# Kernel optimization log

Measured on AMD Instinct MI355X. Metric: run time of the kernel, lower is better.

## Reference

```python
import jax, jax.numpy as jnp
import numpy as np

B, S, C_IN = 32, 4096, 21
D_MODEL = 512
M, TAU = 7, 1
K = M + 1                 # kernel_size = 8
NUM_KERNELS = 74          # 73 depthwise kernels + 1 'final' kernel
PAD = M * TAU             # left zero-pad = 7 -> num_windows == S
PROJ_IN = 73 * C_IN + 1   # 1534


def setup_inputs() -> dict:
    key = jax.random.key(0)
    k_x, k_k, k_w, k_b = jax.random.split(key, 4)
    x = jax.random.normal(k_x, (B, S, C_IN), dtype=jnp.float32)
    kernels = jax.random.normal(k_k, (NUM_KERNELS, K), dtype=jnp.float32)
    # nn.Conv1d(PROJ_IN, D_MODEL, 1): weight [D_MODEL, PROJ_IN, 1] -> squeeze kernel dim
    fan_in = PROJ_IN
    bound = 1.0 / np.sqrt(fan_in)
    proj_w = jax.random.uniform(k_w, (D_MODEL, PROJ_IN), dtype=jnp.float32, minval=-bound, maxval=bound)
    proj_b = jax.random.uniform(k_b, (D_MODEL,), dtype=jnp.float32, minval=-bound, maxval=bound)
    return {"x": x, "kernels": kernels, "proj_w": proj_w, "proj_b": proj_b}


def reference(x, kernels, proj_w, proj_b):
    # x: [B, S, C]. Left-pad the time axis with zeros (ConstantPad1d((PAD, 0), 0)).
    xp = jnp.pad(x, ((0, 0), (PAD, 0), (0, 0)))  # [B, S+PAD, C]
    num_windows = x.shape[1]  # (S+PAD) - K + 1 == S when tau == 1
    # Gather sliding windows: [B, W, K, C]
    idx = jnp.arange(num_windows)[:, None] * TAU + jnp.arange(K)[None, :]
    windows = xp[:, idx, :]
    # 73 depthwise kernels, each applied to every channel. Torch concat order is
    # per-kernel blocks of c_in channels: [k0 c0..cC, k1 c0..cC, ...].
    main = jnp.einsum('bwkc,nk->bwnc', windows, kernels[: NUM_KERNELS - 1])
    main = main.reshape(x.shape[0], num_windows, (NUM_KERNELS - 1) * x.shape[2])
    # Final feature: last kernel applied to one channel (torch uses a random
    # channel; fixed to channel 0 here for determinism).
    final = jnp.einsum('bwk,k->bw', windows[:, :, :, 0], kernels[NUM_KERNELS - 1])[..., None]
    combined = jnp.concatenate([main, final], axis=2)  # [B, W, 73*C+1]
    # 1x1 Conv1d projection over channels -> [B, D_MODEL, W]
    out = jnp.einsum('bwc,dc->bdw', combined, proj_w) + proj_b[None, :, None]
    return out
```

## Files before the change

### kernel.cpp

```cpp
#include <hip/hip_runtime.h>

#define B_    32
#define S_    4096
#define CIN   21
#define DM    512
#define KW    8
#define NK    74
#define PROJIN 1534
#define CP    24
#define KSEG  192

#define WT    256
#define DTB   128
#define SROWS 263
#define R_    265

typedef __attribute__((ext_vector_type(8))) short bf16x8;
typedef __attribute__((ext_vector_type(4))) float f32x4;

__device__ __forceinline__ unsigned short f2bf_rne(float x) {
  unsigned u = __float_as_uint(x);
  unsigned r = (u + 0x7FFFu + ((u >> 16) & 1u)) >> 16;
  return (unsigned short)r;
}
__device__ __forceinline__ float bf2f(unsigned short b) {
  return __uint_as_float(((unsigned)b) << 16);
}

__global__ __launch_bounds__(256) void build_weff(
    const float* __restrict__ kernels, const float* __restrict__ proj_w,
    unsigned short* __restrict__ wh, unsigned short* __restrict__ wl) {
  __shared__ float pw[PROJIN];
  __shared__ float kk[NK * KW];
  const int d = blockIdx.x, tid = threadIdx.x;
  for (int i = tid; i < PROJIN; i += 256) pw[i] = proj_w[d * PROJIN + i];
  for (int i = tid; i < NK * KW; i += 256) kk[i] = kernels[i];
  __syncthreads();
  if (tid < KSEG) {
    const int k = tid / CP, c = tid % CP;
    float acc = 0.f;
    if (c < CIN) {
      #pragma unroll 1
      for (int n = 0; n < 73; ++n)
        acc = fmaf(pw[n * CIN + c], kk[n * KW + k], acc);
      if (c == 0) acc = fmaf(pw[PROJIN - 1], kk[73 * KW + k], acc);
    }
    const unsigned short h = f2bf_rne(acc);
    wh[d * KSEG + tid] = h;
    wl[d * KSEG + tid] = f2bf_rne(acc - bf2f(h));
  }
}

__global__ __launch_bounds__(256, 2) void conv_mfma2(
    const float* __restrict__ x, const unsigned short* __restrict__ wh,
    const unsigned short* __restrict__ wl, const float* __restrict__ proj_b,
    float* __restrict__ out) {
  __shared__ __align__(16) unsigned short Xt[2 * 3 * R_ * 8];

  const int tid = threadIdx.x;
  const int blk = blockIdx.x;
  const int dt = blk & 3;
  const int wt = (blk >> 2) & 15;
  const int b  = blk >> 6;
  const int d0 = dt * DTB;
  const int w0 = wt * WT;

  const float* xb = x + (size_t)b * (S_ * CIN);
  for (int i = tid; i < SROWS * CP; i += 256) {
    const int s = i / CP, c = i - s * CP;
    const int wg = w0 - 7 + s;
    float v = 0.f;
    if (c < CIN && wg >= 0) v = xb[wg * CIN + c];
    const unsigned short h = f2bf_rne(v);
    const unsigned short lo = f2bf_rne(v - bf2f(h));
    const int g = c >> 3, e = c & 7;
    Xt[(g * R_ + s) * 8 + e] = h;
    Xt[((3 + g) * R_ + s) * 8 + e] = lo;
  }
  __syncthreads();

  const int l    = tid & 63;
  const int wave = tid >> 6;
  const int l15  = l & 15;
  const int q    = l >> 4;
  const int q8   = q * 8;

  int koff[6];
  #pragma unroll
  for (int s = 0; s < 6; ++s) {
    const int k0 = 32 * s + q8;
    const int k = k0 / CP, c0 = k0 - k * CP;
    koff[s] = (c0 >> 3) * R_ + k;
  }
  const int rowb = wave * 64 + l15;
  const int wrow = (d0 + l15) * KSEG + q8;

  f32x4 acc[4][8] = {};

  #pragma unroll
  for (int s = 0; s < 6; ++s) {
    bf16x8 fh[4], fl[4];
    #pragma unroll
    for (int m = 0; m < 4; ++m) {
      const int gi = koff[s] + rowb + m * 16;
      fh[m] = *(const bf16x8*)&Xt[gi * 8];
      fl[m] = *(const bf16x8*)&Xt[(gi + 3 * R_) * 8];
    }
    #pragma unroll
    for (int half = 0; half < 2; ++half) {
      bf16x8 fwh[4], fwl[4];
      #pragma unroll
      for (int j = 0; j < 4; ++j) {
        const int n = half * 4 + j;
        const int off = wrow + n * (16 * KSEG) + s * 32;
        fwh[j] = *(const bf16x8*)&wh[off];
        fwl[j] = *(const bf16x8*)&wl[off];
      }
      #pragma unroll
      for (int m = 0; m < 4; ++m)
        #pragma unroll
        for (int j = 0; j < 4; ++j) {
          const int n = half * 4 + j;
          acc[m][n] = __builtin_amdgcn_mfma_f32_16x16x32_bf16(
              fh[m], fwh[j], acc[m][n], 0, 0, 0);
          acc[m][n] = __builtin_amdgcn_mfma_f32_16x16x32_bf16(
              fl[m], fwh[j], acc[m][n], 0, 0, 0);
          acc[m][n] = __builtin_amdgcn_mfma_f32_16x16x32_bf16(
              fh[m], fwl[j], acc[m][n], 0, 0, 0);
        }
    }
  }

  const size_t ob = (size_t)b * DM * S_;
  #pragma unroll
  for (int n = 0; n < 8; ++n) {
    const int d = d0 + n * 16 + l15;
    const float bias = proj_b[d];
    #pragma unroll
    for (int m = 0; m < 4; ++m) {
      const int w = w0 + wave * 64 + m * 16 + q * 4;
      f32x4 v = acc[m][n];
      v = v + bias;
      *(f32x4*)&out[ob + (size_t)d * S_ + w] = v;
    }
  }
}

extern "C" void kernel_launch(void* const* d_in, const int* in_sizes, int n_in,
                              void* d_out, int out_size, void* d_ws, size_t ws_size,
                              hipStream_t stream) {
  const float* x       = (const float*)d_in[0];
  const float* kernels = (const float*)d_in[1];
  const float* proj_w  = (const float*)d_in[2];
  const float* proj_b  = (const float*)d_in[3];
  float* out = (float*)d_out;

  unsigned short* weff_hi = (unsigned short*)d_ws;
  unsigned short* weff_lo = weff_hi + (size_t)DM * KSEG;

  build_weff<<<DM, 256, 0, stream>>>(kernels, proj_w, weff_hi, weff_lo);
  conv_mfma2<<<B_ * 16 * 4, 256, 0, stream>>>(x, weff_hi, weff_lo, proj_b, out);
}
```

Baseline: 418.0 us.

## Pre-split X into bf16 hi/lo image and stream chunks via LDS-direct loads

Adds a separate pass that converts x into a padded bf16 hi/lo, channel-grouped image in global memory, and lays the effective weights out in an LDS-ready tiled image. The conv kernel now uses persistent 512-thread blocks, each owning one batch and 32 output channels. Each block loads its weight tile once and loops over 8 time chunks, fetching each X chunk with global_load_lds so the next chunk's load overlaps the output stores. Blocks are mapped for XCD locality and outputs use nontemporal stores. The extra preprocessing pass writes and rereads a bf16 copy of x. Each block also does less MFMA work per loaded X element, since it now covers 32 instead of 128 output channels.

Measured after the change: 346.8 us. -17.0%, faster.

```diff
diff --git a/kernel.cpp b/kernel.cpp
--- a/kernel.cpp
+++ b/kernel.cpp
@@ -8,36 +8,44 @@
 #define NK    74
 #define PROJIN 1534
 #define CP    24
-#define KSEG  192
 
-#define WT    256
-#define DTB   128
-#define SROWS 263
-#define R_    265
+#define DTB   32
+#define CW    512
+#define NCH   8
+#define ROWCH 519
+#define ROWP  4104
+#define WGRAN 1584
+#define XGRAN (6*ROWCH)
 
 typedef __attribute__((ext_vector_type(8))) short bf16x8;
 typedef __attribute__((ext_vector_type(4))) float f32x4;
 
 __device__ __forceinline__ unsigned short f2bf_rne(float x) {
   unsigned u = __float_as_uint(x);
-  unsigned r = (u + 0x7FFFu + ((u >> 16) & 1u)) >> 16;
-  return (unsigned short)r;
+  return (unsigned short)((u + 0x7FFFu + ((u >> 16) & 1u)) >> 16);
 }
 __device__ __forceinline__ float bf2f(unsigned short b) {
   return __uint_as_float(((unsigned)b) << 16);
 }
 
-__global__ __launch_bounds__(256) void build_weff(
+#define MFMA16 __builtin_amdgcn_mfma_f32_16x16x32_bf16
+#define GLOAD16(gsrc, ldst)                                              \
+  __builtin_amdgcn_global_load_lds(                                      \
+      (const __attribute__((address_space(1))) unsigned int*)(gsrc),     \
+      (__attribute__((address_space(3))) unsigned int*)(ldst), 16, 0, 0)
+
+__global__ __launch_bounds__(256) void build_weff3(
     const float* __restrict__ kernels, const float* __restrict__ proj_w,
-    unsigned short* __restrict__ wh, unsigned short* __restrict__ wl) {
+    unsigned short* __restrict__ wimg) {
   __shared__ float pw[PROJIN];
   __shared__ float kk[NK * KW];
   const int d = blockIdx.x, tid = threadIdx.x;
   for (int i = tid; i < PROJIN; i += 256) pw[i] = proj_w[d * PROJIN + i];
   for (int i = tid; i < NK * KW; i += 256) kk[i] = kernels[i];
   __syncthreads();
-  if (tid < KSEG) {
-    const int k = tid / CP, c = tid % CP;
+  if (tid < 192) {
+    const int kap = tid;
+    const int k = kap / CP, c = kap - k * CP;
     float acc = 0.f;
     if (c < CIN) {
       #pragma unroll 1
@@ -46,102 +54,124 @@
       if (c == 0) acc = fmaf(pw[PROJIN - 1], kk[73 * KW + k], acc);
     }
     const unsigned short h = f2bf_rne(acc);
-    wh[d * KSEG + tid] = h;
-    wl[d * KSEG + tid] = f2bf_rne(acc - bf2f(h));
+    const unsigned short lo = f2bf_rne(acc - bf2f(h));
+    const int s = kap >> 5, q = (kap >> 3) & 3, e = kap & 7;
+    const size_t base = (size_t)(d >> 5) * WGRAN * 8;
+    const int dloc = d & 31;
+    wimg[base + ((size_t)((s * 4 + q) * 33 + dloc)) * 8 + e] = h;
+    wimg[base + ((size_t)(((6 + s) * 4 + q) * 33 + dloc)) * 8 + e] = lo;
   }
 }
 
-__global__ __launch_bounds__(256, 2) void conv_mfma2(
-    const float* __restrict__ x, const unsigned short* __restrict__ wh,
-    const unsigned short* __restrict__ wl, const float* __restrict__ proj_b,
-    float* __restrict__ out) {
-  __shared__ __align__(16) unsigned short Xt[2 * 3 * R_ * 8];
+__global__ __launch_bounds__(256) void build_xt(
+    const float* __restrict__ x, unsigned short* __restrict__ xt) {
+  const int t = blockIdx.x * 256 + threadIdx.x;
+  const int b = t / (6 * ROWP);
+  int rem = t - b * 6 * ROWP;
+  const int pg = rem / ROWP;
+  const int row = rem - pg * ROWP;
+  const int h = pg / 3, g = pg % 3;
+  const int w = row - 7;
+  bf16x8 o;
+  #pragma unroll
+  for (int e = 0; e < 8; ++e) {
+    const int c = g * 8 + e;
+    float v = 0.f;
+    if (w >= 0 && w < S_ && c < CIN) v = x[((size_t)b * S_ + w) * CIN + c];
+    const unsigned short hi = f2bf_rne(v);
+    o[e] = (short)(h ? f2bf_rne(v - bf2f(hi)) : hi);
+  }
+  *(bf16x8*)&xt[(size_t)t * 8] = o;
+}
+
+__global__ __launch_bounds__(512, 4) void conv3(
+    const unsigned short* __restrict__ wimg,
+    const unsigned short* __restrict__ xt,
+    const float* __restrict__ proj_b, float* __restrict__ out) {
+  extern __shared__ __align__(16) char smem[];
+  unsigned short* Xl = (unsigned short*)smem;
+  unsigned short* Wl = (unsigned short*)(smem + XGRAN * 16);
 
   const int tid = threadIdx.x;
-  const int blk = blockIdx.x;
-  const int dt = blk & 3;
-  const int wt = (blk >> 2) & 15;
-  const int b  = blk >> 6;
+  const int p = blockIdx.x;
+  const int xcd = p & 7, slot = p >> 3;
+  const int b = xcd * 4 + (slot >> 4);
+  const int dt = slot & 15;
   const int d0 = dt * DTB;
-  const int w0 = wt * WT;
 
-  const float* xb = x + (size_t)b * (S_ * CIN);
-  for (int i = tid; i < SROWS * CP; i += 256) {
-    const int s = i / CP, c = i - s * CP;
-    const int wg = w0 - 7 + s;
-    float v = 0.f;
-    if (c < CIN && wg >= 0) v = xb[wg * CIN + c];
-    const unsigned short h = f2bf_rne(v);
-    const unsigned short lo = f2bf_rne(v - bf2f(h));
-    const int g = c >> 3, e = c & 7;
-    Xt[(g * R_ + s) * 8 + e] = h;
-    Xt[((3 + g) * R_ + s) * 8 + e] = lo;
+  const unsigned short* wsrc = wimg + (size_t)dt * WGRAN * 8;
+  for (int i = tid; i < WGRAN; i += 512)
+    GLOAD16(wsrc + (size_t)i * 8, Wl + (size_t)i * 8);
+  const unsigned short* xb = xt + (size_t)b * 6 * ROWP * 8;
+  for (int i = tid; i < XGRAN; i += 512) {
+    const int pg = i / ROWCH, r = i - pg * ROWCH;
+    GLOAD16(xb + ((size_t)pg * ROWP + r) * 8, Xl + (size_t)i * 8);
   }
-  __syncthreads();
 
-  const int l    = tid & 63;
-  const int wave = tid >> 6;
-  const int l15  = l & 15;
-  const int q    = l >> 4;
-  const int q8   = q * 8;
+  const int l = tid & 63;
+  const int wg = tid >> 6;
+  const int l15 = l & 15;
+  const int q = l >> 4;
+  const int q8 = q * 8;
 
   int koff[6];
   #pragma unroll
   for (int s = 0; s < 6; ++s) {
     const int k0 = 32 * s + q8;
     const int k = k0 / CP, c0 = k0 - k * CP;
-    koff[s] = (c0 >> 3) * R_ + k;
+    koff[s] = (c0 >> 3) * ROWCH + k;
   }
-  const int rowb = wave * 64 + l15;
-  const int wrow = (d0 + l15) * KSEG + q8;
+  const int xrow = wg * 64 + l15;
+  const int wq = q * 33 + l15;
+  const float bias0 = proj_b[d0 + l15];
+  const float bias1 = proj_b[d0 + 16 + l15];
+  const size_t ob = (size_t)b * DM * S_;
 
-  f32x4 acc[4][8] = {};
+  for (int c = 0; c < NCH; ++c) {
+    asm volatile("s_waitcnt vmcnt(0)" ::: "memory");
+    __syncthreads();
 
-  #pragma unroll
-  for (int s = 0; s < 6; ++s) {
-    bf16x8 fh[4], fl[4];
+    f32x4 acc[4][2] = {};
     #pragma unroll
-    for (int m = 0; m < 4; ++m) {
-      const int gi = koff[s] + rowb + m * 16;
-      fh[m] = *(const bf16x8*)&Xt[gi * 8];
-      fl[m] = *(const bf16x8*)&Xt[(gi + 3 * R_) * 8];
+    for (int s = 0; s < 6; ++s) {
+      const int wgr = s * 132 + wq;
+      const bf16x8 fw0h = *(const bf16x8*)&Wl[(size_t)wgr * 8];
+      const bf16x8 fw1h = *(const bf16x8*)&Wl[(size_t)(wgr + 16) * 8];
+      const bf16x8 fw0l = *(const bf16x8*)&Wl[(size_t)(wgr + 792) * 8];
+      const bf16x8 fw1l = *(const bf16x8*)&Wl[(size_t)(wgr + 808) * 8];
+      #pragma unroll
+      for (int m = 0; m < 4; ++m) {
+        const int xg = koff[s] + xrow + m * 16;
+        const bf16x8 fh = *(const bf16x8*)&Xl[(size_t)xg * 8];
+        const bf16x8 fl = *(const bf16x8*)&Xl[(size_t)(xg + 1557) * 8];
+        acc[m][0] = MFMA16(fh, fw0h, acc[m][0], 0, 0, 0);
+        acc[m][0] = MFMA16(fl, fw0h, acc[m][0], 0, 0, 0);
+        acc[m][0] = MFMA16(fh, fw0l, acc[m][0], 0, 0, 0);
+        acc[m][1] = MFMA16(fh, fw1h, acc[m][1], 0, 0, 0);
+        acc[m][1] = MFMA16(fl, fw1h, acc[m][1], 0, 0, 0);
+        acc[m][1] = MFMA16(fh, fw1l, acc[m][1], 0, 0, 0);
+      }
     }
+    __syncthreads();
+
+    if (c + 1 < NCH) {
+      const size_t cb = (size_t)(c + 1) * CW;
+      for (int i = tid; i < XGRAN; i += 512) {
+        const int pg = i / ROWCH, r = i - pg * ROWCH;
+        GLOAD16(xb + ((size_t)pg * ROWP + cb + r) * 8, Xl + (size_t)i * 8);
+      }
+    }
+
     #pragma unroll
-    for (int half = 0; half < 2; ++half) {
-      bf16x8 fwh[4], fwl[4];
+    for (int nd = 0; nd < 2; ++nd) {
+      const int d = d0 + nd * 16 + l15;
+      const float bias = nd ? bias1 : bias0;
+      float* orow = out + ob + (size_t)d * S_ + c * CW + wg * 64 + q * 4;
       #pragma unroll
-      for (int j = 0; j < 4; ++j) {
-        const int n = half * 4 + j;
-        const int off = wrow + n * (16 * KSEG) + s * 32;
-        fwh[j] = *(const bf16x8*)&wh[off];
-        fwl[j] = *(const bf16x8*)&wl[off];
+      for (int m = 0; m < 4; ++m) {
+        f32x4 v = acc[m][nd] + bias;
+        __builtin_nontemporal_store(v, (f32x4*)(orow + m * 16));
       }
-      #pragma unroll
-      for (int m = 0; m < 4; ++m)
-        #pragma unroll
-        for (int j = 0; j < 4; ++j) {
-          const int n = half * 4 + j;
-          acc[m][n] = __builtin_amdgcn_mfma_f32_16x16x32_bf16(
-              fh[m], fwh[j], acc[m][n], 0, 0, 0);
-          acc[m][n] = __builtin_amdgcn_mfma_f32_16x16x32_bf16(
-              fl[m], fwh[j], acc[m][n], 0, 0, 0);
-          acc[m][n] = __builtin_amdgcn_mfma_f32_16x16x32_bf16(
-              fh[m], fwl[j], acc[m][n], 0, 0, 0);
-        }
-    }
-  }
-
-  const size_t ob = (size_t)b * DM * S_;
-  #pragma unroll
-  for (int n = 0; n < 8; ++n) {
-    const int d = d0 + n * 16 + l15;
-    const float bias = proj_b[d];
-    #pragma unroll
-    for (int m = 0; m < 4; ++m) {
-      const int w = w0 + wave * 64 + m * 16 + q * 4;
-      f32x4 v = acc[m][n];
-      v = v + bias;
-      *(f32x4*)&out[ob + (size_t)d * S_ + w] = v;
     }
   }
 }
@@ -155,9 +185,14 @@
   const float* proj_b  = (const float*)d_in[3];
   float* out = (float*)d_out;
 
-  unsigned short* weff_hi = (unsigned short*)d_ws;
-  unsigned short* weff_lo = weff_hi + (size_t)DM * KSEG;
+  unsigned short* wimg = (unsigned short*)d_ws;
+  unsigned short* xt   = wimg + (size_t)16 * WGRAN * 8;
 
-  build_weff<<<DM, 256, 0, stream>>>(kernels, proj_w, weff_hi, weff_lo);
-  conv_mfma2<<<B_ * 16 * 4, 256, 0, stream>>>(x, weff_hi, weff_lo, proj_b, out);
+  build_weff3<<<DM, 256, 0, stream>>>(kernels, proj_w, wimg);
+  build_xt<<<(B_ * 6 * ROWP) / 256, 256, 0, stream>>>(x, xt);
+
+  (void)hipFuncSetAttribute((const void*)conv3,
+                            hipFuncAttributeMaxDynamicSharedMemorySize,
+                            (XGRAN + WGRAN) * 16);
+  conv3<<<512, 512, (XGRAN + WGRAN) * 16, stream>>>(wimg, xt, proj_b, out);
 }
```
